# Kernel optimization log

Measured on AMD Instinct MI355X. Metric: run time of the kernel, lower is better.

## Reference

```python
import jax, jax.numpy as jnp
import numpy as np

HIDDEN = 4096
NUM_BLOCKS = 8
BLOCK = HIDDEN // NUM_BLOCKS  # 512


def setup_inputs() -> dict:
    key = jax.random.key(0)
    k1, k2, k3, k4 = jax.random.split(key, 4)
    return {
        "weight": jax.random.normal(k1, (HIDDEN, HIDDEN), dtype=jnp.float32) * 0.02,
        "bias": jax.random.normal(k2, (HIDDEN,), dtype=jnp.float32) * 0.02,
        "x": jax.random.normal(k3, (4, 2048, HIDDEN), dtype=jnp.float32),
        "proj_R": jax.random.normal(k4, (NUM_BLOCKS, BLOCK, BLOCK), dtype=jnp.float32) * 0.02,
        "layer_idx": 0,
    }


def _cayley_batch(A):
    # Q = (I - S) @ inv(I + S + 1e-6*I), S = 0.5*(A - A^T), batched over blocks
    r = A.shape[-1]
    I = jnp.eye(r, dtype=A.dtype)
    S = 0.5 * (A - jnp.swapaxes(A, -2, -1))
    Minv = jnp.linalg.inv(I + S + 1e-6 * I)
    return jnp.einsum('bij,bjk->bik', I - S, Minv)


def reference(weight, bias, x, proj_R, layer_idx):
    Q = _cayley_batch(proj_R)                     # [nb, bs, bs], orthogonal blocks
    nb, bs, _ = Q.shape
    # block_diag(Q) @ weight == batched block-row matmul (off-diagonal blocks are zero)
    Wb = weight.reshape(nb, bs, weight.shape[1])  # [nb, bs, in]
    filt = jnp.einsum('bij,bjk->bik', Q, Wb).reshape(nb * bs, weight.shape[1])
    # F.linear(x, filt, bias)
    return jnp.einsum('bsi,oi->bso', x, filt) + bias
```

## Files before the change

kernel.cpp:

```cpp
#include <hip/hip_runtime.h>

typedef unsigned short u16;
typedef __attribute__((ext_vector_type(8))) short bf16x8;
typedef __attribute__((ext_vector_type(4))) float f32x4;
typedef __attribute__((ext_vector_type(8))) unsigned short u16x8;
typedef __attribute__((ext_vector_type(4))) unsigned short u16x4;

__device__ __forceinline__ u16 f2bf(float f){
  unsigned int u = __builtin_bit_cast(unsigned int, f);
  u += 0x7FFFu + ((u >> 16) & 1u);
  return (u16)(u >> 16);
}
__device__ __forceinline__ float bf2f(u16 h){
  unsigned int u = ((unsigned int)h) << 16;
  return __builtin_bit_cast(float, u);
}

__device__ __forceinline__ void load16(const u16* g, u16* s){
  __builtin_amdgcn_global_load_lds((const __attribute__((address_space(1))) unsigned int*)g,
                                   (__attribute__((address_space(3))) unsigned int*)s,
                                   16, 0, 0);
}

__global__ __launch_bounds__(256) void build_s(const float* __restrict__ R, u16* __restrict__ Sbf,
                                               u16* __restrict__ Dbf){
  int idx = blockIdx.x * 256 + threadIdx.x;
  int b = idx >> 18;
  int i = (idx >> 9) & 511;
  int j = idx & 511;
  float a  = R[idx];
  float at = R[(b << 18) + (j << 9) + i];
  float s = 0.5f * (a - at);
  Sbf[idx] = f2bf(s);
  Dbf[idx] = f2bf((i == j ? 2.000003f : 0.0f) - 2.000001f * s);
}

__global__ __launch_bounds__(256) void transpose_w(const float* __restrict__ W, u16* __restrict__ Wt){
  const int b = blockIdx.z;
  const int i0 = blockIdx.x << 5;
  const int j0 = blockIdx.y << 5;
  __shared__ float tile[32][33];
  const int t = threadIdx.x;
  const int r = t >> 3, c = (t & 7) << 2;
  float4 v = *(const float4*)&W[(size_t)((b << 9) + j0 + r) * 4096 + i0 + c];
  tile[r][c+0] = v.x; tile[r][c+1] = v.y; tile[r][c+2] = v.z; tile[r][c+3] = v.w;
  __syncthreads();
  u16x4 o = { f2bf(tile[c+0][r]), f2bf(tile[c+1][r]), f2bf(tile[c+2][r]), f2bf(tile[c+3][r]) };
  *(u16x4*)&Wt[((size_t)b << 21) + (size_t)(i0 + r) * 512 + j0 + c] = o;
}

template<int EPI>
__global__ __launch_bounds__(256) void gemm_ns(const u16* __restrict__ A, const u16* __restrict__ B,
                                               void* __restrict__ Cout, void* __restrict__ aux,
                                               void* __restrict__ aux2,
                                               int M, int N, int K){
  const int bz = blockIdx.z;
  const char* Ab = (const char*)(A + (size_t)bz * M * K);
  const char* Bb = (const char*)(B + (size_t)bz * N * K);
  const int m0 = blockIdx.y << 6, n0 = blockIdx.x << 6;
  __shared__ __align__(16) char As[4096];
  __shared__ __align__(16) char Bs[4096];
  const int t = threadIdx.x;
  const int w = t >> 6, l = t & 63;
  const int wm = w >> 1, wn = w & 1;
  const size_t Kb = (size_t)K << 1;
  const int sR = t >> 2;
  const int sK = ((t ^ (t >> 2)) & 3) << 4;
  const int kq = (((l >> 4) ^ l) & 3) << 4;
  const int aRd = ((wm << 5) + (l & 15)) * 64 + kq;
  const int bRd = ((wn << 5) + (l & 15)) * 64 + kq;
  f32x4 acc[2][2] = {};
  for (int k0 = 0; k0 < K; k0 += 32){
    const size_t kb = (size_t)k0 << 1;
    load16((const u16*)(Ab + (size_t)(m0 + sR) * Kb + kb + sK), (u16*)(As + t * 16));
    load16((const u16*)(Bb + (size_t)(n0 + sR) * Kb + kb + sK), (u16*)(Bs + t * 16));
    __syncthreads();
    bf16x8 aF[2], bF[2];
#pragma unroll
    for (int mf = 0; mf < 2; ++mf) aF[mf] = *(const bf16x8*)(As + aRd + (mf << 10));
#pragma unroll
    for (int nf = 0; nf < 2; ++nf) bF[nf] = *(const bf16x8*)(Bs + bRd + (nf << 10));
#pragma unroll
    for (int mf = 0; mf < 2; ++mf)
#pragma unroll
      for (int nf = 0; nf < 2; ++nf)
        acc[mf][nf] = __builtin_amdgcn_mfma_f32_16x16x32_bf16(aF[mf], bF[nf], acc[mf][nf], 0, 0, 0);
    __syncthreads();
  }
#pragma unroll
  for (int mf = 0; mf < 2; ++mf){
#pragma unroll
    for (int nf = 0; nf < 2; ++nf){
      const int col = n0 + (wn << 5) + (nf << 4) + (l & 15);
#pragma unroll
      for (int q = 0; q < 4; ++q){
        const int row = m0 + (wm << 5) + (mf << 4) + ((l >> 4) << 2) + q;
        float v = acc[mf][nf][q];
        size_t gi = ((size_t)bz * M + row) * N + col;
        size_t g2 = (((size_t)bz * M + row) << 10) + col;
        if (EPI == 2){
          ((u16*)Cout)[gi] = f2bf(v);
        } else if (EPI == 3){
          ((u16*)Cout)[gi] = f2bf((row == col ? 2.0f : 0.0f) - v);
        } else if (EPI == 9){
          ((u16*)Cout)[gi] = f2bf(v - (row == col ? 1.0f : 0.0f));
        } else {
          float p = v + (row == col ? 1.000002f : 0.0f);
          u16 ph = f2bf(p);
          ((u16*)Cout)[g2] = ph;
          ((u16*)Cout)[g2 + 512] = f2bf(p - bf2f(ph));
          const float beta = 0.8264463f;
          u16 x1 = f2bf((row == col ? 2.0f * beta : 0.0f) - beta * beta * p);
          ((u16*)aux)[gi] = x1;
          ((u16*)aux2)[g2] = x1;
          ((u16*)aux2)[g2 + 512] = x1;
        }
      }
    }
  }
}

template<int EPI>
__global__ __launch_bounds__(512, 2) void gemm256(const u16* __restrict__ A, const u16* __restrict__ B,
                                                  void* __restrict__ Cout, const float* __restrict__ aux,
                                                  int M, int N, int K){
  __shared__ __align__(16) char lds[131072];
  const int bz = blockIdx.z;
  const char* Ab = (const char*)(A + (size_t)bz * M * K);
  const char* Bb = (const char*)(B + (size_t)bz * N * K);
  const int NB = N >> 8;
  const int nwg = gridDim.x;
  const int bid = blockIdx.x;
  const int swzb = (bid & 7) * (nwg >> 3) + (bid >> 3);
  const int m0 = (swzb / NB) << 8;
  const int n0 = (swzb % NB) << 8;
  const int tid = threadIdx.x;
  const int w = tid >> 6, l = tid & 63;
  const int wm = w >> 2, wn = w & 3;
  const size_t Kb = (size_t)K << 1;
  const int NT = K >> 6;
  const int sRow = tid >> 3;
  const int sCol = ((tid & 7) << 4) ^ ((sRow & 7) << 4);
  const int sDst = tid << 4;
  const char* aS = Ab + (size_t)(m0 + sRow) * Kb + sCol;
  const char* bS = Bb + (size_t)(n0 + sRow) * Kb + sCol;
  const int lrow = (l & 15) << 7;
  const int kq0 = (((l >> 4) << 4)) ^ ((l & 7) << 4);
  const int aOff = (wm << 14) + lrow;
  const int bOff = 32768 + ((wn >> 1) << 14) + ((wn & 1) << 13) + lrow;

#define STAGE_H(isB, h, tt) { \
    const int _lo = (((tt) & 1) << 16) + ((isB) << 15) + ((h) << 14); \
    const char* _s = ((isB) ? bS : aS) + ((size_t)((h) << 7)) * Kb + ((size_t)(tt) << 7); \
    load16((const u16*)_s, (u16*)(lds + _lo + sDst)); \
    load16((const u16*)(_s + (Kb << 6)), (u16*)(lds + _lo + 8192 + sDst)); }

#define RD_A(bufb, UQ) \
  _Pragma("unroll") for (int i2 = 0; i2 < 4; ++i2){ \
    aF[i2][0] = *(const bf16x8*)(lds + (bufb) + aOff + ((UQ) << 13) + (i2 << 11) + kq0); \
    aF[i2][1] = *(const bf16x8*)(lds + (bufb) + aOff + ((UQ) << 13) + (i2 << 11) + (kq0 ^ 64)); }

#define RD_B(bufb, VQ) \
  _Pragma("unroll") for (int j2 = 0; j2 < 2; ++j2){ \
    bF[VQ][j2][0] = *(const bf16x8*)(lds + (bufb) + bOff + ((VQ) << 12) + (j2 << 11) + kq0); \
    bF[VQ][j2][1] = *(const bf16x8*)(lds + (bufb) + bOff + ((VQ) << 12) + (j2 << 11) + (kq0 ^ 64)); }

#define MFMA16(UQ, VQ) \
    _Pragma("unroll") for (int i2 = 0; i2 < 4; ++i2) \
      _Pragma("unroll") for (int j2 = 0; j2 < 2; ++j2){ \
        acc[(UQ)*4+i2][(VQ)*2+j2] = __builtin_amdgcn_mfma_f32_16x16x32_bf16(aF[i2][0], bF[VQ][j2][0], acc[(UQ)*4+i2][(VQ)*2+j2], 0, 0, 0); \
        acc[(UQ)*4+i2][(VQ)*2+j2] = __builtin_amdgcn_mfma_f32_16x16x32_bf16(aF[i2][1], bF[VQ][j2][1], acc[(UQ)*4+i2][(VQ)*2+j2], 0, 0, 0); }

#define BAR asm volatile("s_barrier" ::: "memory");
#define VM0 asm volatile("s_waitcnt vmcnt(0)" ::: "memory");

  bf16x8 aF[4][2], bF[2][2][2];
  f32x4 acc[8][4] = {};

  STAGE_H(0,0,0) STAGE_H(1,0,0) STAGE_H(0,1,0) STAGE_H(1,1,0)
  VM0 BAR

#define KTILE(t, bufb) { \
    RD_A(bufb, 0) RD_B(bufb, 0) \
    if ((t) + 1 < NT) { STAGE_H(0,0,(t)+1) STAGE_H(1,0,(t)+1) } \
    MFMA16(0,0) \
    RD_B(bufb, 1) \
    if ((t) + 1 < NT) { STAGE_H(0,1,(t)+1) STAGE_H(1,1,(t)+1) } \
    MFMA16(0,1) \
    RD_A(bufb, 1) \
    MFMA16(1,1) \
    MFMA16(1,0) \
    __builtin_amdgcn_sched_barrier(0); \
    VM0 BAR }

#pragma unroll 1
  for (int tp = 0; tp < NT; tp += 2){
    KTILE(tp, 0)
    KTILE(tp+1, 65536)
  }
#undef KTILE

#pragma unroll
  for (int mf = 0; mf < 8; ++mf){
#pragma unroll
    for (int nf = 0; nf < 4; ++nf){
      const int col = n0 + (wn << 6) + (nf << 4) + (l & 15);
#pragma unroll
      for (int q = 0; q < 4; ++q){
        const int row = m0 + (wm << 7) + (mf << 4) + ((l >> 4) << 2) + q;
        float v = acc[mf][nf][q];
        if (EPI == 0){
          ((float*)Cout)[(size_t)row * N + col] = v + aux[col];
        } else {
          ((u16*)Cout)[((size_t)bz * M + row) * N + col] = f2bf(v);
        }
      }
    }
  }
#undef STAGE_H
#undef RD_A
#undef RD_B
#undef MFMA16
#undef BAR
#undef VM0
}

__global__ __launch_bounds__(512, 2) void gemm256f(const float* __restrict__ Af, const u16* __restrict__ Bw,
                                                   float* __restrict__ Cout, const float* __restrict__ bias,
                                                   int M, int N, int K){
  __shared__ __align__(16) char lds[131072];
  const char* Bb = (const char*)Bw;
  const int NB = N >> 8;
  const int nwg = gridDim.x;
  const int bid = blockIdx.x;
  const int swzb = (bid & 7) * (nwg >> 3) + (bid >> 3);
  const int m0 = (swzb / NB) << 8;
  const int n0 = (swzb % NB) << 8;
  const int tid = threadIdx.x;
  const int w = tid >> 6, l = tid & 63;
  const int wm = w >> 2, wn = w & 3;
  const size_t Kb = (size_t)K << 1;
  const int NT = K >> 6;
  const int sRow = tid >> 3;
  const int sCol = ((tid & 7) << 4) ^ ((sRow & 7) << 4);
  const int sDst = tid << 4;
  const char* bS = Bb + (size_t)(n0 + sRow) * Kb + sCol;
  const float* aS = Af + (size_t)(m0 + sRow) * K + (sCol >> 1);
  const size_t rowK64 = (size_t)64 * K;
  const int lrow = (l & 15) << 7;
  const int kq0 = (((l >> 4) << 4)) ^ ((l & 7) << 4);
  const int aOff = (wm << 14) + lrow;
  const int bOff = 32768 + ((wn >> 1) << 14) + ((wn & 1) << 13) + lrow;

#define STAGE_B(h, tt) { \
    const int _lo = (((tt) & 1) << 16) + 32768 + ((h) << 14); \
    const char* _s = bS + ((size_t)((h) << 7)) * Kb + ((size_t)(tt) << 7); \
    load16((const u16*)_s, (u16*)(lds + _lo + sDst)); \
    load16((const u16*)(_s + (Kb << 6)), (u16*)(lds + _lo + 8192 + sDst)); }

#define A_ISSUE(p, tt) { \
    const float* _a = aS + (size_t)(tt) * 64 + (size_t)((p) << 1) * rowK64; \
    sa0 = *(const float4*)(_a);           sb0 = *(const float4*)(_a + 4); \
    sa1 = *(const float4*)(_a + rowK64);  sb1 = *(const float4*)(_a + rowK64 + 4); }
#define A_WRITE(p, tt) { \
    const int _lo = (((tt) & 1) << 16) + ((p) << 14); \
    u16x8 o0 = { f2bf(sa0.x), f2bf(sa0.y), f2bf(sa0.z), f2bf(sa0.w), \
                 f2bf(sb0.x), f2bf(sb0.y), f2bf(sb0.z), f2bf(sb0.w) }; \
    *(u16x8*)(lds + _lo + sDst) = o0; \
    u16x8 o1 = { f2bf(sa1.x), f2bf(sa1.y), f2bf(sa1.z), f2bf(sa1.w), \
                 f2bf(sb1.x), f2bf(sb1.y), f2bf(sb1.z), f2bf(sb1.w) }; \
    *(u16x8*)(lds + _lo + 8192 + sDst) = o1; }

#define RD_A(bufb, UQ) \
  _Pragma("unroll") for (int i2 = 0; i2 < 4; ++i2){ \
    aF[i2][0] = *(const bf16x8*)(lds + (bufb) + aOff + ((UQ) << 13) + (i2 << 11) + kq0); \
    aF[i2][1] = *(const bf16x8*)(lds + (bufb) + aOff + ((UQ) << 13) + (i2 << 11) + (kq0 ^ 64)); }

#define RD_B(bufb, VQ) \
  _Pragma("unroll") for (int j2 = 0; j2 < 2; ++j2){ \
    bF[VQ][j2][0] = *(const bf16x8*)(lds + (bufb) + bOff + ((VQ) << 12) + (j2 << 11) + kq0); \
    bF[VQ][j2][1] = *(const bf16x8*)(lds + (bufb) + bOff + ((VQ) << 12) + (j2 << 11) + (kq0 ^ 64)); }

#define MFMA16(UQ, VQ) \
    _Pragma("unroll") for (int i2 = 0; i2 < 4; ++i2) \
      _Pragma("unroll") for (int j2 = 0; j2 < 2; ++j2){ \
        acc[(UQ)*4+i2][(VQ)*2+j2] = __builtin_amdgcn_mfma_f32_16x16x32_bf16(aF[i2][0], bF[VQ][j2][0], acc[(UQ)*4+i2][(VQ)*2+j2], 0, 0, 0); \
        acc[(UQ)*4+i2][(VQ)*2+j2] = __builtin_amdgcn_mfma_f32_16x16x32_bf16(aF[i2][1], bF[VQ][j2][1], acc[(UQ)*4+i2][(VQ)*2+j2], 0, 0, 0); }

#define BAR asm volatile("s_barrier" ::: "memory");
#define LGK0 asm volatile("s_waitcnt lgkmcnt(0)" ::: "memory");
#define VM0 asm volatile("s_waitcnt vmcnt(0)" ::: "memory");

  bf16x8 aF[4][2], bF[2][2][2];
  float4 sa0, sb0, sa1, sb1;
  f32x4 acc[8][4] = {};

  A_ISSUE(0, 0) STAGE_B(0, 0) STAGE_B(1, 0)
  A_WRITE(0, 0)
  A_ISSUE(1, 0)
  A_WRITE(1, 0)
  LGK0 VM0 BAR

#define KTILE(t, bufb) { \
    if ((t) + 1 < NT) { A_ISSUE(0, (t)+1) STAGE_B(0, (t)+1) } \
    RD_A(bufb, 0) RD_B(bufb, 0) \
    MFMA16(0,0) \
    RD_B(bufb, 1) \
    if ((t) + 1 < NT) { STAGE_B(1, (t)+1) } \
    MFMA16(0,1) \
    if ((t) + 1 < NT) { A_WRITE(0, (t)+1) A_ISSUE(1, (t)+1) } \
    RD_A(bufb, 1) \
    MFMA16(1,1) \
    MFMA16(1,0) \
    if ((t) + 1 < NT) { A_WRITE(1, (t)+1) } \
    __builtin_amdgcn_sched_barrier(0); \
    LGK0 VM0 BAR }

#pragma unroll 1
  for (int tp = 0; tp < NT; tp += 2){
    KTILE(tp, 0)
    KTILE(tp+1, 65536)
  }
#undef KTILE

#pragma unroll
  for (int mf = 0; mf < 8; ++mf){
#pragma unroll
    for (int nf = 0; nf < 4; ++nf){
      const int col = n0 + (wn << 6) + (nf << 4) + (l & 15);
#pragma unroll
      for (int q = 0; q < 4; ++q){
        const int row = m0 + (wm << 7) + (mf << 4) + ((l >> 4) << 2) + q;
        Cout[(size_t)row * N + col] = acc[mf][nf][q] + bias[col];
      }
    }
  }
#undef STAGE_B
#undef A_ISSUE
#undef A_WRITE
#undef RD_A
#undef RD_B
#undef MFMA16
#undef BAR
#undef LGK0
#undef VM0
}

extern "C" void kernel_launch(void* const* d_in, const int* in_sizes, int n_in,
                              void* d_out, int out_size, void* d_ws, size_t ws_size,
                              hipStream_t stream){
  const float* W    = (const float*)d_in[0];
  const float* bias = (const float*)d_in[1];
  const float* x    = (const float*)d_in[2];
  const float* R    = (const float*)d_in[3];
  (void)in_sizes; (void)n_in; (void)out_size; (void)ws_size;

  char* ws = (char*)d_ws;
  const size_t MiB = (size_t)1 << 20;
  u16*   Sbf  = (u16*)(ws + 0 * MiB);
  u16*   Dbf  = (u16*)(ws + 4 * MiB);
  u16*   X1   = (u16*)(ws + 16 * MiB);
  u16*   Ybf  = (u16*)(ws + 20 * MiB);
  u16*   X2   = (u16*)(ws + 24 * MiB);
  u16*   Phl  = (u16*)(ws + 28 * MiB);
  u16*   X1d  = (u16*)(ws + 44 * MiB);
  u16*   G    = Sbf;
  u16*   Wt   = (u16*)(ws + 8 * MiB);
  u16*   filt = (u16*)(ws + 64 * MiB);

  const dim3 gNS(8, 8, 8);

  build_s<<<8192, 256, 0, stream>>>(R, Sbf, Dbf);
  gemm_ns<11><<<gNS, 256, 0, stream>>>(Sbf, Sbf, Phl, X1, X1d, 512, 512, 512);
  gemm_ns<3><<<gNS, 256, 0, stream>>>(Phl, X1d, Ybf, nullptr, nullptr, 512, 512, 1024);
  gemm_ns<2><<<gNS, 256, 0, stream>>>(X1, Ybf, X2, nullptr, nullptr, 512, 512, 512);
  gemm_ns<9><<<gNS, 256, 0, stream>>>(Dbf, X2, G, nullptr, nullptr, 512, 512, 512);
  transpose_w<<<dim3(128, 16, 8), 256, 0, stream>>>(W, Wt);
  gemm256<2><<<dim3(32, 1, 8), 512, 0, stream>>>(G, Wt, (void*)filt, nullptr, 512, 4096, 512);
  gemm256f<<<dim3(512, 1, 1), 512, 0, stream>>>(x, filt, (float*)d_out, bias, 8192, 4096, 4096);
}
```

Before: 422.1 us.

## Prefetch fp32 A tiles two K-steps ahead into double-buffered registers

```diff
diff --git a/kernel.cpp b/kernel.cpp
--- a/kernel.cpp
+++ b/kernel.cpp
@@ -14,6 +14,11 @@
 __device__ __forceinline__ float bf2f(u16 h){
   unsigned int u = ((unsigned int)h) << 16;
   return __builtin_bit_cast(float, u);
+}
+__device__ __forceinline__ u16x8 cvt8(float4 a, float4 b){
+  u16x8 o = { f2bf(a.x), f2bf(a.y), f2bf(a.z), f2bf(a.w),
+              f2bf(b.x), f2bf(b.y), f2bf(b.z), f2bf(b.w) };
+  return o;
 }
 
 __device__ __forceinline__ void load16(const u16* g, u16* s){
@@ -258,18 +263,19 @@
     load16((const u16*)_s, (u16*)(lds + _lo + sDst)); \
     load16((const u16*)(_s + (Kb << 6)), (u16*)(lds + _lo + 8192 + sDst)); }
 
-#define A_ISSUE(p, tt) { \
-    const float* _a = aS + (size_t)(tt) * 64 + (size_t)((p) << 1) * rowK64; \
-    sa0 = *(const float4*)(_a);           sb0 = *(const float4*)(_a + 4); \
-    sa1 = *(const float4*)(_a + rowK64);  sb1 = *(const float4*)(_a + rowK64 + 4); }
-#define A_WRITE(p, tt) { \
-    const int _lo = (((tt) & 1) << 16) + ((p) << 14); \
-    u16x8 o0 = { f2bf(sa0.x), f2bf(sa0.y), f2bf(sa0.z), f2bf(sa0.w), \
-                 f2bf(sb0.x), f2bf(sb0.y), f2bf(sb0.z), f2bf(sb0.w) }; \
-    *(u16x8*)(lds + _lo + sDst) = o0; \
-    u16x8 o1 = { f2bf(sa1.x), f2bf(sa1.y), f2bf(sa1.z), f2bf(sa1.w), \
-                 f2bf(sb1.x), f2bf(sb1.y), f2bf(sb1.z), f2bf(sb1.w) }; \
-    *(u16x8*)(lds + _lo + 8192 + sDst) = o1; }
+#define A_ISSUE(S, tt) if ((tt) < NT) { \
+    const float* _a = aS + (size_t)(tt) * 64; \
+    S##0 = *(const float4*)(_a);               S##1 = *(const float4*)(_a + 4); \
+    S##2 = *(const float4*)(_a + rowK64);      S##3 = *(const float4*)(_a + rowK64 + 4); \
+    S##4 = *(const float4*)(_a + 2*rowK64);    S##5 = *(const float4*)(_a + 2*rowK64 + 4); \
+    S##6 = *(const float4*)(_a + 3*rowK64);    S##7 = *(const float4*)(_a + 3*rowK64 + 4); }
+
+#define A_WRITE(S, tt) if ((tt) < NT) { \
+    const int _lo = (((tt) & 1) << 16); \
+    *(u16x8*)(lds + _lo +         sDst) = cvt8(S##0, S##1); \
+    *(u16x8*)(lds + _lo +  8192 + sDst) = cvt8(S##2, S##3); \
+    *(u16x8*)(lds + _lo + 16384 + sDst) = cvt8(S##4, S##5); \
+    *(u16x8*)(lds + _lo + 24576 + sDst) = cvt8(S##6, S##7); }
 
 #define RD_A(bufb, UQ) \
   _Pragma("unroll") for (int i2 = 0; i2 < 4; ++i2){ \
@@ -292,34 +298,34 @@
 #define VM0 asm volatile("s_waitcnt vmcnt(0)" ::: "memory");
 
   bf16x8 aF[4][2], bF[2][2][2];
-  float4 sa0, sb0, sa1, sb1;
+  float4 p0, p1, p2, p3, p4, p5, p6, p7;
+  float4 q0, q1, q2, q3, q4, q5, q6, q7;
   f32x4 acc[8][4] = {};
 
-  A_ISSUE(0, 0) STAGE_B(0, 0) STAGE_B(1, 0)
-  A_WRITE(0, 0)
-  A_ISSUE(1, 0)
-  A_WRITE(1, 0)
+  A_ISSUE(p, 0) A_ISSUE(q, 1)
+  STAGE_B(0, 0) STAGE_B(1, 0)
+  A_WRITE(p, 0)
   LGK0 VM0 BAR
 
-#define KTILE(t, bufb) { \
-    if ((t) + 1 < NT) { A_ISSUE(0, (t)+1) STAGE_B(0, (t)+1) } \
+#define KTILE(t, bufb, Siss, Swr) { \
+    A_ISSUE(Siss, (t)+2) \
     RD_A(bufb, 0) RD_B(bufb, 0) \
+    if ((t) + 1 < NT) { STAGE_B(0, (t)+1) } \
     MFMA16(0,0) \
     RD_B(bufb, 1) \
     if ((t) + 1 < NT) { STAGE_B(1, (t)+1) } \
     MFMA16(0,1) \
-    if ((t) + 1 < NT) { A_WRITE(0, (t)+1) A_ISSUE(1, (t)+1) } \
     RD_A(bufb, 1) \
     MFMA16(1,1) \
     MFMA16(1,0) \
-    if ((t) + 1 < NT) { A_WRITE(1, (t)+1) } \
+    A_WRITE(Swr, (t)+1) \
     __builtin_amdgcn_sched_barrier(0); \
     LGK0 VM0 BAR }
 
 #pragma unroll 1
   for (int tp = 0; tp < NT; tp += 2){
-    KTILE(tp, 0)
-    KTILE(tp+1, 65536)
+    KTILE(tp, 0, p, q)
+    KTILE(tp+1, 65536, q, p)
   }
 #undef KTILE
 
```

After: 915.9 us. 117% more time.
